# Optimization experiments

Measured on AMD Instinct MI355X. Metric: run time of the kernel, lower is better.

## Reference

```python
import jax, jax.numpy as jnp
import numpy as np

BSZ, L, P, H = 8, 8192, 128, 128


def setup_inputs() -> dict:
    key = jax.random.key(0)
    ks = jax.random.split(key, 7)
    x = jax.random.normal(ks[0], (BSZ, L, H), jnp.float32)
    A_diag = jax.random.uniform(ks[1], (P,), jnp.float32, 0.0, 2.0)
    G_diag = jax.random.uniform(ks[2], (P,), jnp.float32, 0.0, 1.0)
    dt = jax.random.normal(ks[3], (P,), jnp.float32)
    B = jax.random.uniform(ks[4], (P, H, 2), jnp.float32, -1.0, 1.0) / np.sqrt(H)
    C = jax.random.uniform(ks[5], (H, P, 2), jnp.float32, -1.0, 1.0) / np.sqrt(P)
    D = jax.random.normal(ks[6], (H,), jnp.float32)
    return {"x": x, "A_diag": A_diag, "G_diag": G_diag, "dt": dt, "B": B, "C": C, "D": D}


def _project_G(G, A, dt):
    # clamp G >= 0 and fold A into the valid stability interval [A_low, A_high]
    G = jnp.maximum(G, 0.0)
    dt2 = jnp.maximum(dt ** 2, 1e-06)
    s = jnp.sqrt(1.0 + dt * G)
    A_low = (2.0 + dt * G - 2.0 * s) / dt2
    A_high = (2.0 + dt * G + 2.0 * s) / dt2
    A_proj = A_low + jax.nn.relu(A - A_low) - jax.nn.relu(A - A_high)
    return A_proj, G


def _binop(q_i, q_j):
    # 2x2 block (per diagonal state p) recurrence composition: M_j @ M_i
    A_i, b_i = q_i
    A_j, b_j = q_j
    A_new = jnp.einsum('...ikp,...kjp->...ijp', A_j, A_i)
    b_new = jnp.einsum('...ikp,...kp->...ip', A_j, b_i) + b_j
    return A_new, b_new


def reference(x, A_diag, G_diag, dt, B, C, D):
    # _project_A_dt
    dt_s = jax.nn.sigmoid(dt)                       # (P,)
    A = jnp.maximum(A_diag, 0.0)
    # G_base = projected G given (A, dt)
    _, G_base = _project_G(G_diag, A, dt_s)
    # constant damping: G_seq is G_base broadcast over time, then re-projected per step
    G_seq = jnp.broadcast_to(G_base, (L, P))        # (L,P)
    A_seq, G_seq = _project_G(G_seq, A, dt_s)       # broadcasts over L
    A_fin = jnp.min(A_seq, axis=0)                  # (P,)
    # complex input projection Bu_k = B_complex @ u_k
    Bc = B[..., 0] + 1j * B[..., 1]                 # (P,H)
    Cc = C[..., 0] + 1j * C[..., 1]                 # (H,P)
    Bu = jnp.einsum('blh,ph->blp', x, Bc)           # (BSZ,L,P) complex64
    # IMEX transition coefficients
    S = 1.0 + dt_s * G_seq                          # (L,P)
    M11 = 1.0 / S
    M12 = -(dt_s / S) * A_fin
    M21 = dt_s / S
    M22 = 1.0 - (dt_s ** 2 / S) * A_fin
    M = jnp.stack([jnp.stack([M11, M12], axis=-2),
                   jnp.stack([M21, M22], axis=-2)], axis=-3)   # (L,2,2,P) real
    F = jnp.stack([(dt_s / S) * Bu, (dt_s ** 2 / S) * Bu], axis=-2)  # (BSZ,L,2,P) complex
    M_b = jnp.broadcast_to(M, (BSZ,) + M.shape)     # (BSZ,L,2,2,P)
    _, xs = jax.lax.associative_scan(_binop, (M_b, F), axis=1)
    ys = xs[..., 1, :]                              # (BSZ,L,P) complex: x-component
    out = jnp.einsum('blp,hp->blh', ys, Cc).real + D * x
    return out
```

## Files before the change

kernel.cpp:

```cpp
#include <hip/hip_runtime.h>
#include <math.h>

#define BSZ_ 8
#define LEN_ 8192
#define NC_  128
#define CT_  64

typedef __attribute__((ext_vector_type(8))) short bf16x8;
typedef __attribute__((ext_vector_type(4))) float f32x4;
typedef __attribute__((ext_vector_type(4))) unsigned short u16x4;
typedef __attribute__((ext_vector_type(8))) unsigned short u16x8;

#define OFF_PRM 0
#define OFF_W1T 2048
#define OFF_W2T (OFF_W1T + 16384)
#define OFF_MPW (OFF_W2T + 16384)
#define OFF_SUM (OFF_MPW + 16384)
#define OFF_V2  (OFF_SUM + 524288)

__device__ __forceinline__ unsigned short f2bf(float f) {
    unsigned u = __builtin_bit_cast(unsigned, f);
    u += 0x7fffu + ((u >> 16) & 1u);
    return (unsigned short)(u >> 16);
}

__device__ __forceinline__ unsigned short f2bf_fast(float f) {
    unsigned u = __builtin_bit_cast(unsigned, f);
    return (unsigned short)((u + 0x8000u) >> 16);
}

__device__ __forceinline__ float bf2f(unsigned short u) {
    return __builtin_bit_cast(float, (unsigned)u << 16);
}

__global__ __launch_bounds__(256) void k_setup(const float* __restrict__ A_diag,
                                               const float* __restrict__ G_diag,
                                               const float* __restrict__ dt,
                                               const float* __restrict__ B,
                                               const float* __restrict__ C,
                                               float* __restrict__ ws)
{
    int i = blockIdx.x * 256 + threadIdx.x;
    {
        int pc = i >> 7, h = i & 127;
        int p = pc >> 1, cc = pc & 1;
        float dts = 1.f / (1.f + expf(-dt[p]));
        float G = fmaxf(G_diag[p], 0.f);
        float c1 = dts / (1.f + dts * G);
        ((unsigned short*)(ws + OFF_W1T))[i] = f2bf(c1 * B[p * 256 + h * 2 + cc]);
    }
    {
        float v = C[i];
        ((unsigned short*)(ws + OFF_W2T))[i] = f2bf((i & 1) ? -v : v);
    }
    if (i < 8192) {
        int k = (i >> 7) + 1;
        int p = i & 127;
        float dtv = dt[p];
        float dts = 1.f / (1.f + expf(-dtv));
        float A   = fmaxf(A_diag[p], 0.f);
        float G   = fmaxf(G_diag[p], 0.f);
        float dt2 = fmaxf(dts * dts, 1e-6f);
        float s   = sqrtf(1.f + dts * G);
        float A_low  = (2.f + dts * G - 2.f * s) / dt2;
        float A_high = (2.f + dts * G + 2.f * s) / dt2;
        float Af = A_low + fmaxf(A - A_low, 0.f) - fmaxf(A - A_high, 0.f);
        float S   = 1.f + dts * G;
        float M11 = 1.f / S;
        float M12 = -(dts / S) * Af;
        float M21 = dts / S;
        float M22 = 1.f - (dts * dts / S) * Af;

        float r11 = 1.f, r12 = 0.f, r21 = 0.f, r22 = 1.f;
        float b11 = M11, b12 = M12, b21 = M21, b22 = M22;
        int kk = k;
#pragma unroll
        for (int it = 0; it < 7; ++it) {
            if (kk & 1) {
                float t11 = b11 * r11 + b12 * r21;
                float t12 = b11 * r12 + b12 * r22;
                float t21 = b21 * r11 + b22 * r21;
                float t22 = b21 * r12 + b22 * r22;
                r11 = t11; r12 = t12; r21 = t21; r22 = t22;
            }
            float s11 = b11 * b11 + b12 * b21;
            float s12 = b11 * b12 + b12 * b22;
            float s21 = b21 * b11 + b22 * b21;
            float s22 = b21 * b12 + b22 * b22;
            b11 = s11; b12 = s12; b21 = s21; b22 = s22;
            kk >>= 1;
        }
        {
            int tq = (k - 1) >> 2, j = (k - 1) & 3;
            ((float2*)(ws + OFF_MPW))[((size_t)tq * 128 + p) * 4 + j] =
                make_float2(r21, r22);
        }

        float* prm = ws + OFF_PRM + p * 16;
        if (k == 1) {
            prm[0] = M11; prm[1] = M12; prm[2] = M21; prm[3] = M22; prm[4] = dts;
        }
        if (k == 64) {
            prm[5] = r11; prm[6] = r12; prm[7] = r21; prm[8] = r22;
            float u11 = r11, u12 = r12, u21 = r21, u22 = r22;
#pragma unroll
            for (int it = 0; it < 4; ++it) {
                float s11 = u11 * u11 + u12 * u21;
                float s12 = u11 * u12 + u12 * u22;
                float s21 = u21 * u11 + u22 * u21;
                float s22 = u21 * u12 + u22 * u22;
                u11 = s11; u12 = s12; u21 = s21; u22 = s22;
            }
            prm[9] = u11; prm[10] = u12; prm[11] = u21; prm[12] = u22;
        }
    }
}

__device__ __forceinline__ void stage_x(const float* __restrict__ X, size_t row0,
                                        int tid, unsigned short (*xs)[136])
{
    int r = tid >> 4, cl = (tid & 15) * 8;
#pragma unroll
    for (int i = 0; i < 4; ++i) {
        int rr = r + i * 16;
        const float* src = X + (row0 + rr) * 128 + cl;
        float4 v0 = *(const float4*)src;
        float4 v1 = *(const float4*)(src + 4);
        unsigned short* dst = &xs[rr][cl];
        dst[0] = f2bf_fast(v0.x); dst[1] = f2bf_fast(v0.y); dst[2] = f2bf_fast(v0.z); dst[3] = f2bf_fast(v0.w);
        dst[4] = f2bf_fast(v1.x); dst[5] = f2bf_fast(v1.y); dst[6] = f2bf_fast(v1.z); dst[7] = f2bf_fast(v1.w);
    }
}

__device__ __forceinline__ void gemm1_acc(const unsigned short (*xs)[136],
                                          const unsigned short* __restrict__ W1T,
                                          int wv, int lane, f32x4 acc[4][4])
{
    int l15 = lane & 15, quad = lane >> 4;
    int nbase = wv * 64;
#pragma unroll
    for (int kk = 0; kk < 4; ++kk) {
        int k0 = kk * 32 + quad * 8;
        bf16x8 af[4], bg[4];
#pragma unroll
        for (int mi = 0; mi < 4; ++mi) af[mi] = *(const bf16x8*)&xs[mi * 16 + l15][k0];
#pragma unroll
        for (int nj = 0; nj < 4; ++nj)
            bg[nj] = *(const bf16x8*)(W1T + (size_t)(nbase + nj * 16 + l15) * 128 + k0);
#pragma unroll
        for (int mi = 0; mi < 4; ++mi)
#pragma unroll
            for (int nj = 0; nj < 4; ++nj)
                acc[mi][nj] = __builtin_amdgcn_mfma_f32_16x16x32_bf16(af[mi], bg[nj], acc[mi][nj], 0, 0, 0);
    }
}

__global__ __launch_bounds__(256) void k_fuse1(const float* __restrict__ X,
                                               float* __restrict__ ws)
{
    __shared__ __align__(16) char smem[32 * 260 * 4];
    unsigned short (*xs)[136] = (unsigned short (*)[136])smem;
    float (*fl)[260] = (float (*)[260])smem;

    int tid = threadIdx.x;
    int bc = blockIdx.x;
    int b = bc >> 7, c = bc & 127;
    size_t row0 = (size_t)b * LEN_ + (size_t)c * CT_;

    stage_x(X, row0, tid, xs);
    __syncthreads();

    int wv = tid >> 6, lane = tid & 63;
    int l15 = lane & 15, quad = lane >> 4, nbase = wv * 64;
    f32x4 acc[4][4] = {};
    gemm1_acc(xs, (const unsigned short*)(ws + OFF_W1T), wv, lane, acc);
    __syncthreads();

    const float* prm = ws + OFF_PRM + (tid >> 1) * 16;
    float M11 = prm[0], M12 = prm[1], dts = prm[4];
    u16x4* V2q = (u16x4*)(ws + OFF_V2) + (size_t)bc * 4096;
    float h1 = 0.f, h2 = 0.f;

#pragma unroll
    for (int half = 0; half < 2; ++half) {
#pragma unroll
        for (int mi = 0; mi < 2; ++mi)
#pragma unroll
            for (int nj = 0; nj < 4; ++nj)
#pragma unroll
                for (int r = 0; r < 4; ++r)
                    fl[mi * 16 + quad * 4 + r][nbase + nj * 16 + l15] =
                        acc[half * 2 + mi][nj][r];
        __syncthreads();
#pragma unroll
        for (int g = 0; g < 8; ++g) {
            u16x4 pk;
#pragma unroll
            for (int i = 0; i < 4; ++i) {
                float u = fl[g * 4 + i][tid];
                float n1 = fmaf(M11, h1, fmaf(M12, h2, u));
                float n2 = fmaf(dts, n1, h2);
                h1 = n1; h2 = n2;
                pk[i] = f2bf_fast(h2);
            }
            V2q[(half * 8 + g) * 256 + tid] = pk;
        }
        __syncthreads();
    }
    *(float2*)(ws + OFF_SUM + (((size_t)bc) * 256 + tid) * 2) = make_float2(h1, h2);
}

__global__ __launch_bounds__(256) void k_scan2(float* __restrict__ ws)
{
    __shared__ float2 sums[32][8];
    int blk = blockIdx.x;
    int b = blk >> 3, chb = (blk & 7) * 32;
    int tid = threadIdx.x;
    int chl = tid & 31, seg = tid >> 5;
    int ch = chb + chl;
    const float* prm = ws + OFF_PRM + (ch >> 1) * 16;
    float T11 = prm[5], T12 = prm[6], T21 = prm[7], T22 = prm[8];
    float U11 = prm[9], U12 = prm[10], U21 = prm[11], U22 = prm[12];
    float* base = ws + OFF_SUM + (size_t)b * 65536 + ch * 2;

    float l1[16], l2[16];
    float s1 = 0.f, s2 = 0.f;
#pragma unroll
    for (int j = 0; j < 16; ++j) {
        float2 l = *(const float2*)(base + (size_t)(seg * 16 + j) * 512);
        l1[j] = l.x; l2[j] = l.y;
        float n1 = fmaf(T11, s1, fmaf(T12, s2, l.x));
        float n2 = fmaf(T21, s1, fmaf(T22, s2, l.y));
        s1 = n1; s2 = n2;
    }
    sums[chl][seg] = make_float2(s1, s2);
    __syncthreads();

    if (tid < 32) {
        float e1 = 0.f, e2 = 0.f;
#pragma unroll
        for (int k = 0; k < 8; ++k) {
            float2 t = sums[tid][k];
            sums[tid][k] = make_float2(e1, e2);
            float n1 = fmaf(U11, e1, fmaf(U12, e2, t.x));
            float n2 = fmaf(U21, e1, fmaf(U22, e2, t.y));
            e1 = n1; e2 = n2;
        }
    }
    __syncthreads();

    float2 E = sums[chl][seg];
    float e1 = E.x, e2 = E.y;
#pragma unroll
    for (int j = 0; j < 16; ++j) {
        *(float2*)(base + (size_t)(seg * 16 + j) * 512) = make_float2(e1, e2);
        float n1 = fmaf(T11, e1, fmaf(T12, e2, l1[j]));
        float n2 = fmaf(T21, e1, fmaf(T22, e2, l2[j]));
        e1 = n1; e2 = n2;
    }
}

__global__ __launch_bounds__(256) void k_fuse2(const float* __restrict__ X,
                                               const float* __restrict__ Dv,
                                               float* __restrict__ ws,
                                               float* __restrict__ out)
{
    __shared__ __align__(16) unsigned short ysb[64][264];

    int tid = threadIdx.x;
    int bc = blockIdx.x;
    int b = bc >> 7, c = bc & 127;
    size_t row0 = (size_t)b * LEN_ + (size_t)c * CT_;

    {
        int q = tid & 127;
        int tseg = tid >> 7;
        float4 Cp = *(const float4*)(ws + OFF_SUM + ((size_t)bc * 256 + 2 * q) * 2);
        const unsigned short* V2b = (const unsigned short*)(ws + OFF_V2) +
                                    (size_t)bc * 16384;
        const float2* MPW = (const float2*)(ws + OFF_MPW);
#pragma unroll
        for (int g = 0; g < 8; ++g) {
            int tq = tseg * 8 + g;
            u16x8 v = *(const u16x8*)(V2b + (size_t)tq * 1024 + 8 * q);
            const float2* MP = MPW + ((size_t)tq * 128 + q) * 4;
            float4 mA = *(const float4*)MP;
            float4 mB = *(const float4*)(MP + 2);
            int t0 = tq * 4;
            float y0, y1;
            y0 = fmaf(mA.x, Cp.x, fmaf(mA.y, Cp.y, bf2f(v[0])));
            y1 = fmaf(mA.x, Cp.z, fmaf(mA.y, Cp.w, bf2f(v[4])));
            *(ushort2*)&ysb[t0 + 0][2 * q] = make_ushort2(f2bf_fast(y0), f2bf_fast(y1));
            y0 = fmaf(mA.z, Cp.x, fmaf(mA.w, Cp.y, bf2f(v[1])));
            y1 = fmaf(mA.z, Cp.z, fmaf(mA.w, Cp.w, bf2f(v[5])));
            *(ushort2*)&ysb[t0 + 1][2 * q] = make_ushort2(f2bf_fast(y0), f2bf_fast(y1));
            y0 = fmaf(mB.x, Cp.x, fmaf(mB.y, Cp.y, bf2f(v[2])));
            y1 = fmaf(mB.x, Cp.z, fmaf(mB.y, Cp.w, bf2f(v[6])));
            *(ushort2*)&ysb[t0 + 2][2 * q] = make_ushort2(f2bf_fast(y0), f2bf_fast(y1));
            y0 = fmaf(mB.z, Cp.x, fmaf(mB.w, Cp.y, bf2f(v[3])));
            y1 = fmaf(mB.z, Cp.z, fmaf(mB.w, Cp.w, bf2f(v[7])));
            *(ushort2*)&ysb[t0 + 3][2 * q] = make_ushort2(f2bf_fast(y0), f2bf_fast(y1));
        }
    }
    __syncthreads();

    int wv = tid >> 6, lane = tid & 63;
    int l15 = lane & 15, quad = lane >> 4;
    int mrow = (wv & 1) * 32, ncol = (wv >> 1) * 64;
    f32x4 a2[2][4] = {};
    const unsigned short* W2T = (const unsigned short*)(ws + OFF_W2T);
#pragma unroll
    for (int kk = 0; kk < 8; ++kk) {
        int k0 = kk * 32 + quad * 8;
        bf16x8 af[2], bg[4];
#pragma unroll
        for (int mi = 0; mi < 2; ++mi) af[mi] = *(const bf16x8*)&ysb[mrow + mi * 16 + l15][k0];
#pragma unroll
        for (int nj = 0; nj < 4; ++nj)
            bg[nj] = *(const bf16x8*)(W2T + (size_t)(ncol + nj * 16 + l15) * 256 + k0);
#pragma unroll
        for (int mi = 0; mi < 2; ++mi)
#pragma unroll
            for (int nj = 0; nj < 4; ++nj)
                a2[mi][nj] = __builtin_amdgcn_mfma_f32_16x16x32_bf16(af[mi], bg[nj], a2[mi][nj], 0, 0, 0);
    }

#pragma unroll
    for (int mi = 0; mi < 2; ++mi)
#pragma unroll
        for (int nj = 0; nj < 4; ++nj) {
            int col = ncol + nj * 16 + l15;
            float d = Dv[col];
#pragma unroll
            for (int r = 0; r < 4; ++r) {
                size_t gr = row0 + mrow + mi * 16 + quad * 4 + r;
                float xv = X[gr * 128 + col];
                out[gr * 128 + col] = fmaf(d, xv, a2[mi][nj][r]);
            }
        }
}

extern "C" void kernel_launch(void* const* d_in, const int* in_sizes, int n_in,
                              void* d_out, int out_size, void* d_ws, size_t ws_size,
                              hipStream_t stream) {
    const float* x      = (const float*)d_in[0];
    const float* A_diag = (const float*)d_in[1];
    const float* G_diag = (const float*)d_in[2];
    const float* dt     = (const float*)d_in[3];
    const float* B      = (const float*)d_in[4];
    const float* C      = (const float*)d_in[5];
    const float* Dv     = (const float*)d_in[6];
    float* out = (float*)d_out;
    float* ws  = (float*)d_ws;

    k_setup<<<128, 256, 0, stream>>>(A_diag, G_diag, dt, B, C, ws);
    k_fuse1<<<BSZ_ * NC_, 256, 0, stream>>>(x, ws);
    k_scan2<<<64, 256, 0, stream>>>(ws);
    k_fuse2<<<BSZ_ * NC_, 256, 0, stream>>>(x, Dv, ws, out);
}
```

Measured before the change: 133.8 us.

## Fuse chunk-sum scan into last block of fuse1; vectorize stores in staging and epilogue

Removes the separate scan kernel launch by having each fuse1 block publish its chunk-end state with atomic stores and bump a per-batch counter. The last block to finish for a batch then performs the inter-chunk scan for all 256 channels serially over 8 channel groups. The fuse2 epilogue now stages MFMA results through shared memory so the D*x add and output writes use coalesced float4 accesses, and x staging writes packed 16-byte vectors to LDS. The trade-off is that 8 single blocks carry the whole scan with less parallelism than the old 64-block kernel, in exchange for one fewer launch and no launch gap.

```diff
diff --git a/kernel.cpp b/kernel.cpp
--- a/kernel.cpp
+++ b/kernel.cpp
@@ -10,6 +10,7 @@
 typedef __attribute__((ext_vector_type(4))) float f32x4;
 typedef __attribute__((ext_vector_type(4))) unsigned short u16x4;
 typedef __attribute__((ext_vector_type(8))) unsigned short u16x8;
+typedef unsigned long long ulong64;
 
 #define OFF_PRM 0
 #define OFF_W1T 2048
@@ -17,6 +18,7 @@
 #define OFF_MPW (OFF_W2T + 16384)
 #define OFF_SUM (OFF_MPW + 16384)
 #define OFF_V2  (OFF_SUM + 524288)
+#define OFF_CNT (OFF_V2 + 8388608)
 
 __device__ __forceinline__ unsigned short f2bf(float f) {
     unsigned u = __builtin_bit_cast(unsigned, f);
@@ -31,6 +33,17 @@
 
 __device__ __forceinline__ float bf2f(unsigned short u) {
     return __builtin_bit_cast(float, (unsigned)u << 16);
+}
+
+__device__ __forceinline__ void pub8(ulong64* a, float x, float y) {
+    float2 v = make_float2(x, y);
+    __hip_atomic_store(a, __builtin_bit_cast(ulong64, v),
+                       __ATOMIC_RELAXED, __HIP_MEMORY_SCOPE_AGENT);
+}
+__device__ __forceinline__ float2 rd8(const ulong64* a) {
+    ulong64 v = __hip_atomic_load((ulong64*)a, __ATOMIC_RELAXED,
+                                  __HIP_MEMORY_SCOPE_AGENT);
+    return __builtin_bit_cast(float2, v);
 }
 
 __global__ __launch_bounds__(256) void k_setup(const float* __restrict__ A_diag,
@@ -53,6 +66,8 @@
         float v = C[i];
         ((unsigned short*)(ws + OFF_W2T))[i] = f2bf((i & 1) ? -v : v);
     }
+    if (i < 8) ((unsigned*)(ws + OFF_CNT))[i] = 0u;
+
     if (i < 8192) {
         int k = (i >> 7) + 1;
         int p = i & 127;
@@ -126,9 +141,12 @@
         const float* src = X + (row0 + rr) * 128 + cl;
         float4 v0 = *(const float4*)src;
         float4 v1 = *(const float4*)(src + 4);
-        unsigned short* dst = &xs[rr][cl];
-        dst[0] = f2bf_fast(v0.x); dst[1] = f2bf_fast(v0.y); dst[2] = f2bf_fast(v0.z); dst[3] = f2bf_fast(v0.w);
-        dst[4] = f2bf_fast(v1.x); dst[5] = f2bf_fast(v1.y); dst[6] = f2bf_fast(v1.z); dst[7] = f2bf_fast(v1.w);
+        u16x8 pk;
+        pk[0] = f2bf_fast(v0.x); pk[1] = f2bf_fast(v0.y);
+        pk[2] = f2bf_fast(v0.z); pk[3] = f2bf_fast(v0.w);
+        pk[4] = f2bf_fast(v1.x); pk[5] = f2bf_fast(v1.y);
+        pk[6] = f2bf_fast(v1.z); pk[7] = f2bf_fast(v1.w);
+        *(u16x8*)&xs[rr][cl] = pk;
     }
 }
 
@@ -159,6 +177,7 @@
                                                float* __restrict__ ws)
 {
     __shared__ __align__(16) char smem[32 * 260 * 4];
+    __shared__ int lastdone;
     unsigned short (*xs)[136] = (unsigned short (*)[136])smem;
     float (*fl)[260] = (float (*)[260])smem;
 
@@ -207,56 +226,61 @@
         }
         __syncthreads();
     }
-    *(float2*)(ws + OFF_SUM + (((size_t)bc) * 256 + tid) * 2) = make_float2(h1, h2);
-}
-
-__global__ __launch_bounds__(256) void k_scan2(float* __restrict__ ws)
-{
-    __shared__ float2 sums[32][8];
-    int blk = blockIdx.x;
-    int b = blk >> 3, chb = (blk & 7) * 32;
-    int tid = threadIdx.x;
+
+    ulong64* SUM = (ulong64*)(ws + OFF_SUM);
+    pub8(&SUM[(size_t)bc * 256 + tid], h1, h2);
+    __threadfence();
+    if (tid == 0)
+        lastdone = (atomicAdd(&((unsigned*)(ws + OFF_CNT))[b], 1u) == NC_ - 1);
+    __syncthreads();
+    if (!lastdone) return;
+
+    __threadfence();
+    float2 (*sums)[8] = (float2 (*)[8])smem;
     int chl = tid & 31, seg = tid >> 5;
-    int ch = chb + chl;
-    const float* prm = ws + OFF_PRM + (ch >> 1) * 16;
-    float T11 = prm[5], T12 = prm[6], T21 = prm[7], T22 = prm[8];
-    float U11 = prm[9], U12 = prm[10], U21 = prm[11], U22 = prm[12];
-    float* base = ws + OFF_SUM + (size_t)b * 65536 + ch * 2;
-
-    float l1[16], l2[16];
-    float s1 = 0.f, s2 = 0.f;
-#pragma unroll
-    for (int j = 0; j < 16; ++j) {
-        float2 l = *(const float2*)(base + (size_t)(seg * 16 + j) * 512);
-        l1[j] = l.x; l2[j] = l.y;
-        float n1 = fmaf(T11, s1, fmaf(T12, s2, l.x));
-        float n2 = fmaf(T21, s1, fmaf(T22, s2, l.y));
-        s1 = n1; s2 = n2;
-    }
-    sums[chl][seg] = make_float2(s1, s2);
-    __syncthreads();
-
-    if (tid < 32) {
-        float e1 = 0.f, e2 = 0.f;
-#pragma unroll
-        for (int k = 0; k < 8; ++k) {
-            float2 t = sums[tid][k];
-            sums[tid][k] = make_float2(e1, e2);
-            float n1 = fmaf(U11, e1, fmaf(U12, e2, t.x));
-            float n2 = fmaf(U21, e1, fmaf(U22, e2, t.y));
+    ulong64* base0 = SUM + (size_t)b * (NC_ * 256);
+#pragma unroll 1
+    for (int cg = 0; cg < 8; ++cg) {
+        int ch = cg * 32 + chl;
+        const float* pr2 = ws + OFF_PRM + (ch >> 1) * 16;
+        float T11 = pr2[5], T12 = pr2[6], T21 = pr2[7], T22 = pr2[8];
+        float U11 = pr2[9], U12 = pr2[10], U21 = pr2[11], U22 = pr2[12];
+        ulong64* base = base0 + ch;
+
+        float s1 = 0.f, s2 = 0.f;
+#pragma unroll
+        for (int j = 0; j < 16; ++j) {
+            float2 l = rd8(&base[(size_t)(seg * 16 + j) * 256]);
+            float n1 = fmaf(T11, s1, fmaf(T12, s2, l.x));
+            float n2 = fmaf(T21, s1, fmaf(T22, s2, l.y));
+            s1 = n1; s2 = n2;
+        }
+        sums[chl][seg] = make_float2(s1, s2);
+        __syncthreads();
+        if (tid < 32) {
+            float e1 = 0.f, e2 = 0.f;
+#pragma unroll
+            for (int k = 0; k < 8; ++k) {
+                float2 t = sums[tid][k];
+                sums[tid][k] = make_float2(e1, e2);
+                float n1 = fmaf(U11, e1, fmaf(U12, e2, t.x));
+                float n2 = fmaf(U21, e1, fmaf(U22, e2, t.y));
+                e1 = n1; e2 = n2;
+            }
+        }
+        __syncthreads();
+        float2 E = sums[chl][seg];
+        float e1 = E.x, e2 = E.y;
+#pragma unroll
+        for (int j = 0; j < 16; ++j) {
+            size_t idx = (size_t)(seg * 16 + j) * 256;
+            float2 l = rd8(&base[idx]);
+            *(float2*)&base[idx] = make_float2(e1, e2);
+            float n1 = fmaf(T11, e1, fmaf(T12, e2, l.x));
+            float n2 = fmaf(T21, e1, fmaf(T22, e2, l.y));
             e1 = n1; e2 = n2;
         }
-    }
-    __syncthreads();
-
-    float2 E = sums[chl][seg];
-    float e1 = E.x, e2 = E.y;
-#pragma unroll
-    for (int j = 0; j < 16; ++j) {
-        *(float2*)(base + (size_t)(seg * 16 + j) * 512) = make_float2(e1, e2);
-        float n1 = fmaf(T11, e1, fmaf(T12, e2, l1[j]));
-        float n2 = fmaf(T21, e1, fmaf(T22, e2, l2[j]));
-        e1 = n1; e2 = n2;
+        __syncthreads();
     }
 }
 
@@ -265,7 +289,9 @@
                                                float* __restrict__ ws,
                                                float* __restrict__ out)
 {
-    __shared__ __align__(16) unsigned short ysb[64][264];
+    __shared__ __align__(16) char ysmem[64 * 264 * 2];
+    unsigned short (*ysb)[264] = (unsigned short (*)[264])ysmem;
+    float (*fo)[132] = (float (*)[132])ysmem;
 
     int tid = threadIdx.x;
     int bc = blockIdx.x;
@@ -324,20 +350,35 @@
             for (int nj = 0; nj < 4; ++nj)
                 a2[mi][nj] = __builtin_amdgcn_mfma_f32_16x16x32_bf16(af[mi], bg[nj], a2[mi][nj], 0, 0, 0);
     }
+    __syncthreads();
 
 #pragma unroll
     for (int mi = 0; mi < 2; ++mi)
 #pragma unroll
-        for (int nj = 0; nj < 4; ++nj) {
-            int col = ncol + nj * 16 + l15;
-            float d = Dv[col];
-#pragma unroll
-            for (int r = 0; r < 4; ++r) {
-                size_t gr = row0 + mrow + mi * 16 + quad * 4 + r;
-                float xv = X[gr * 128 + col];
-                out[gr * 128 + col] = fmaf(d, xv, a2[mi][nj][r]);
-            }
-        }
+        for (int nj = 0; nj < 4; ++nj)
+#pragma unroll
+            for (int r = 0; r < 4; ++r)
+                fo[mrow + mi * 16 + quad * 4 + r][ncol + nj * 16 + l15] = a2[mi][nj][r];
+    __syncthreads();
+
+    {
+        int colq = tid & 31;
+        int rbase = tid >> 5;
+        float4 dv = *(const float4*)(Dv + colq * 4);
+#pragma unroll
+        for (int k = 0; k < 8; ++k) {
+            int row = rbase + 8 * k;
+            float4 v = *(const float4*)&fo[row][colq * 4];
+            const float* xp = X + (row0 + row) * 128 + colq * 4;
+            float4 xv = *(const float4*)xp;
+            float4 o;
+            o.x = fmaf(dv.x, xv.x, v.x);
+            o.y = fmaf(dv.y, xv.y, v.y);
+            o.z = fmaf(dv.z, xv.z, v.z);
+            o.w = fmaf(dv.w, xv.w, v.w);
+            *(float4*)(out + (row0 + row) * 128 + colq * 4) = o;
+        }
+    }
 }
 
 extern "C" void kernel_launch(void* const* d_in, const int* in_sizes, int n_in,
@@ -355,6 +396,5 @@
 
     k_setup<<<128, 256, 0, stream>>>(A_diag, G_diag, dt, B, C, ws);
     k_fuse1<<<BSZ_ * NC_, 256, 0, stream>>>(x, ws);
-    k_scan2<<<64, 256, 0, stream>>>(ws);
     k_fuse2<<<BSZ_ * NC_, 256, 0, stream>>>(x, Dv, ws, out);
 }
```

Result: slower. 279.9 us (+109.2%).
